# Kernel optimization log

Measured on AMD Instinct MI355X. Metric: run time of the kernel, lower is better.

## Reference

```python
import jax, jax.numpy as jnp
import numpy as np

B, T, I, H, OUT, L = 256, 1200, 16, 128, 1, 2


def _lstm_layer(x, W_ih, W_hh, b_ih, b_hh):
    # x: [B, T, Din]; W_ih: [4H, Din]; W_hh: [4H, H]
    # Precompute input contribution for all timesteps (one big GEMM),
    # then scan only the recurrent part.
    pre = jnp.einsum('btd,gd->btg', x, W_ih) + b_ih + b_hh  # [B, T, 4H]
    pre = jnp.swapaxes(pre, 0, 1)  # [T, B, 4H]
    h0 = jnp.zeros((x.shape[0], W_hh.shape[1]), dtype=x.dtype)
    c0 = jnp.zeros_like(h0)

    def step(carry, p_t):
        h, c = carry
        g = p_t + h @ W_hh.T  # [B, 4H]
        i, f, gg, o = jnp.split(g, 4, axis=-1)  # torch gate order: i, f, g, o
        i = jax.nn.sigmoid(i)
        f = jax.nn.sigmoid(f)
        gg = jnp.tanh(gg)
        o = jax.nn.sigmoid(o)
        c = f * c + i * gg
        h = o * jnp.tanh(c)
        return (h, c), h

    (_, _), hs = jax.lax.scan(step, (h0, c0), pre)  # hs: [T, B, H]
    return jnp.swapaxes(hs, 0, 1)  # [B, T, H]


def setup_inputs() -> dict:
    key = jax.random.key(0)
    ks = jax.random.split(key, 12)
    s = 0.08  # small init scale to keep gates unsaturated
    inp = {
        'x': jax.random.normal(ks[0], (B, T, I), dtype=jnp.float32),
        'W_ih0': jax.random.normal(ks[1], (4 * H, I), dtype=jnp.float32) * s,
        'W_hh0': jax.random.normal(ks[2], (4 * H, H), dtype=jnp.float32) * s,
        'b_ih0': jax.random.normal(ks[3], (4 * H,), dtype=jnp.float32) * s,
        'b_hh0': jax.random.normal(ks[4], (4 * H,), dtype=jnp.float32) * s,
        'W_ih1': jax.random.normal(ks[5], (4 * H, H), dtype=jnp.float32) * s,
        'W_hh1': jax.random.normal(ks[6], (4 * H, H), dtype=jnp.float32) * s,
        'b_ih1': jax.random.normal(ks[7], (4 * H,), dtype=jnp.float32) * s,
        'b_hh1': jax.random.normal(ks[8], (4 * H,), dtype=jnp.float32) * s,
        'W_lin': jax.random.normal(ks[9], (OUT, H), dtype=jnp.float32) * s,
        'b_lin': jax.random.normal(ks[10], (OUT,), dtype=jnp.float32) * s,
    }
    return inp


def reference(x, W_ih0, W_hh0, b_ih0, b_hh0, W_ih1, W_hh1, b_ih1, b_hh1, W_lin, b_lin):
    h1 = _lstm_layer(x, W_ih0, W_hh0, b_ih0, b_hh0)   # [B, T, H]
    h2 = _lstm_layer(h1, W_ih1, W_hh1, b_ih1, b_hh1)  # [B, T, H]
    out = jax.nn.relu(h2)
    out = jnp.einsum('bth,oh->bto', out, W_lin) + b_lin  # [B, T, OUT]
    return out.reshape(-1, 12)  # [B*T*OUT/12, 12]
```

## Files before the change

kernel.cpp:

```cpp
#include <hip/hip_runtime.h>
#include <hip/hip_fp16.h>

#define B_ 256
#define T_ 1200
#define I_ 16
#define H_ 128
#define NT_ (T_ / 8)

typedef __attribute__((ext_vector_type(2))) _Float16 h2;
typedef __attribute__((ext_vector_type(8))) _Float16 f16x8;

union f16x8u { f16x8 v; h2 h[4]; _Float16 s[8]; };

#if __has_builtin(__builtin_amdgcn_fdot2)
__device__ __forceinline__ float fdot2(h2 a, h2 b, float c) {
  return __builtin_amdgcn_fdot2(a, b, c, false);
}
#else
__device__ __forceinline__ float fdot2(h2 a, h2 b, float c) {
  return fmaf((float)a.x, (float)b.x, fmaf((float)a.y, (float)b.y, c));
}
#endif

template <int PAT>
__device__ __forceinline__ float qbcast(float x) {
  return __int_as_float(__builtin_amdgcn_update_dpp(0, __float_as_int(x), PAT, 0xF, 0xF, true));
}

__device__ __forceinline__ float wred(float x) {
  x += __int_as_float(__builtin_amdgcn_update_dpp(0, __float_as_int(x), 0x141, 0xF, 0xF, true));
  x += __int_as_float(__builtin_amdgcn_update_dpp(0, __float_as_int(x), 0x140, 0xF, 0xF, true));
  x += __shfl_xor(x, 16);
  x += __shfl_xor(x, 32);
  return x;
}

__device__ __forceinline__ float sigm(float x) {
  return __builtin_amdgcn_rcpf(1.f + __expf(-x));
}
__device__ __forceinline__ float tanh_(float x) {
  return 1.f - 2.f * __builtin_amdgcn_rcpf(1.f + __expf(2.f * x));
}

__device__ __forceinline__ void load_row_h2(const float* __restrict__ p, h2* w) {
#pragma unroll
  for (int i = 0; i < 32; ++i) {
    const float4 v = *(const float4*)(p + 4 * i);
    w[2 * i].x     = (_Float16)v.x; w[2 * i].y     = (_Float16)v.y;
    w[2 * i + 1].x = (_Float16)v.z; w[2 * i + 1].y = (_Float16)v.w;
  }
}

__global__ __launch_bounds__(512, 2) void k1_layer0(
    const float* __restrict__ xin,
    const float* __restrict__ Wih0, const float* __restrict__ Whh0,
    const float* __restrict__ bih0, const float* __restrict__ bhh0,
    __half* __restrict__ h0ws)
{
  __shared__ __align__(16) __half xs[T_ * I_];
  __shared__ __align__(16) __half hb[2][H_];

  const int tid = threadIdx.x;
  const int q = tid & 3;
  const int j = tid >> 2;
  const int g = q * H_ + j;
  const int b = blockIdx.x;

  {
    const float4* xg4 = (const float4*)(xin + (size_t)b * T_ * I_);
    for (int idx = tid; idx < T_ * I_ / 4; idx += 512) {
      const float4 v = xg4[idx];
      xs[4 * idx]     = __float2half(v.x);
      xs[4 * idx + 1] = __float2half(v.y);
      xs[4 * idx + 2] = __float2half(v.z);
      xs[4 * idx + 3] = __float2half(v.w);
    }
  }

  h2 wh[64], wx[8];
  load_row_h2(Whh0 + (size_t)g * H_, wh);
  {
    const float* px = Wih0 + (size_t)g * I_;
#pragma unroll
    for (int i = 0; i < 4; ++i) {
      const float4 v = *(const float4*)(px + 4 * i);
      wx[2 * i].x     = (_Float16)v.x; wx[2 * i].y     = (_Float16)v.y;
      wx[2 * i + 1].x = (_Float16)v.z; wx[2 * i + 1].y = (_Float16)v.w;
    }
  }
  const float bs = bih0[g] + bhh0[g];
  const float s0 = (q == 2) ? 1.f : 0.f;
  const float s1 = (q == 2) ? -2.f : 1.f;
  const float s2 = (q == 2) ? 2.f : -1.f;

  if (tid < H_) hb[0][tid] = __float2half(0.f);
  float cst = 0.f;
  __half* h0o = h0ws + (size_t)b * T_ * H_ + j;
  __syncthreads();

#pragma unroll 2
  for (int t = 0; t < T_; ++t) {
    const int rb = t & 1;
    float a0 = 0.f, a1 = 0.f, a2 = 0.f, a3 = 0.f;
#pragma unroll
    for (int i = 0; i < 16; ++i) {
      f16x8u u; u.v = *(const f16x8*)(&hb[rb][8 * i]);
      a0 = fdot2(wh[4 * i],     u.h[0], a0);
      a1 = fdot2(wh[4 * i + 1], u.h[1], a1);
      a2 = fdot2(wh[4 * i + 2], u.h[2], a2);
      a3 = fdot2(wh[4 * i + 3], u.h[3], a3);
    }
#pragma unroll
    for (int m = 0; m < 2; ++m) {
      f16x8u u; u.v = *(const f16x8*)(&xs[t * I_ + 8 * m]);
      a0 = fdot2(wx[4 * m],     u.h[0], a0);
      a1 = fdot2(wx[4 * m + 1], u.h[1], a1);
      a2 = fdot2(wx[4 * m + 2], u.h[2], a2);
      a3 = fdot2(wx[4 * m + 3], u.h[3], a3);
    }
    const float pre = (a0 + a1) + (a2 + a3) + bs;
    const float act = fmaf(s1, __builtin_amdgcn_rcpf(1.f + __expf(s2 * pre)), s0);
    const float ig = qbcast<0x00>(act);
    const float fg = qbcast<0x55>(act);
    const float gg = qbcast<0xAA>(act);
    const float og = qbcast<0xFF>(act);
    cst = fg * cst + ig * gg;
    const float hv = og * tanh_(cst);
    const __half hh = __float2half(hv);
    if (q == 0) {
      hb[rb ^ 1][j] = hh;
      h0o[(size_t)t * H_] = hh;
    }
    __syncthreads();
  }
}

__global__ __attribute__((amdgpu_waves_per_eu(4, 4)))
__launch_bounds__(1024) void kb_layer1(
    const __half* __restrict__ h0ws,
    const float* __restrict__ Wih1, const float* __restrict__ Whh1,
    const float* __restrict__ bih1, const float* __restrict__ bhh1,
    const float* __restrict__ Wlin, const float* __restrict__ blin,
    float* __restrict__ out)
{
  __shared__ __align__(16) __half h0til[2][8 * H_];
  __shared__ __align__(16) float aih[2][512];
  __shared__ __align__(16) __half h1b[2][H_];
  __shared__ __align__(16) float red[2][8];

  const int tid = threadIdx.x;
  const bool isA = tid < 512;
  const int lid = tid & 511;
  const int q = lid & 3;
  const int j = lid >> 2;
  const int g = q * H_ + j;
  const int b = blockIdx.x;

  h2 w[64];
  load_row_h2((isA ? Wih1 : Whh1) + (size_t)g * H_, w);

  const float bs = bih1[g] + bhh1[g];
  const float wl = Wlin[j];
  const float bl = blin[0];
  const float s0 = (q == 2) ? 1.f : 0.f;
  const float s1 = (q == 2) ? -2.f : 1.f;
  const float s2 = (q == 2) ? 2.f : -1.f;

  const uint* h0u = (const uint*)(h0ws + (size_t)b * T_ * H_);

  if (isA) ((uint*)h0til[0])[lid] = h0u[lid];
  if (!isA && lid < H_) h1b[0][lid] = __float2half(0.f);
  __syncthreads();
  if (isA) {
    float a0 = 0.f, a1 = 0.f, a2 = 0.f, a3 = 0.f;
#pragma unroll
    for (int i = 0; i < 16; ++i) {
      f16x8u u; u.v = *(const f16x8*)(&h0til[0][8 * i]);
      a0 = fdot2(w[4 * i],     u.h[0], a0);
      a1 = fdot2(w[4 * i + 1], u.h[1], a1);
      a2 = fdot2(w[4 * i + 2], u.h[2], a2);
      a3 = fdot2(w[4 * i + 3], u.h[3], a3);
    }
    aih[0][lid] = (a0 + a1) + (a2 + a3);
  }
  __syncthreads();

  float cst = 0.f;
  uint stg = 0;
  float* op = out + (size_t)b * T_;

  for (int t = 0; t < T_; ++t) {
    const int rb = t & 1;
    if (isA) {
      if ((t & 7) == 0) {
        const int m1 = (t >> 3) + 1;
        if (m1 < NT_) stg = h0u[m1 * 512 + lid];
      }
      const int tt = t + 1;
      if (tt < T_) {
        const __half* hsrc = &h0til[(tt >> 3) & 1][(tt & 7) * H_];
        float a0 = 0.f, a1 = 0.f, a2 = 0.f, a3 = 0.f;
#pragma unroll
        for (int i = 0; i < 16; ++i) {
          f16x8u u; u.v = *(const f16x8*)(hsrc + 8 * i);
          a0 = fdot2(w[4 * i],     u.h[0], a0);
          a1 = fdot2(w[4 * i + 1], u.h[1], a1);
          a2 = fdot2(w[4 * i + 2], u.h[2], a2);
          a3 = fdot2(w[4 * i + 3], u.h[3], a3);
        }
        aih[tt & 1][lid] = (a0 + a1) + (a2 + a3);
      }
      if ((t & 7) == 6) {
        const int m1 = (t >> 3) + 1;
        if (m1 < NT_) ((uint*)h0til[m1 & 1])[lid] = stg;
      }
    } else {
      float a0 = 0.f, a1 = 0.f, a2 = 0.f, a3 = 0.f;
#pragma unroll
      for (int i = 0; i < 16; ++i) {
        f16x8u u; u.v = *(const f16x8*)(&h1b[rb][8 * i]);
        a0 = fdot2(w[4 * i],     u.h[0], a0);
        a1 = fdot2(w[4 * i + 1], u.h[1], a1);
        a2 = fdot2(w[4 * i + 2], u.h[2], a2);
        a3 = fdot2(w[4 * i + 3], u.h[3], a3);
      }
      const float pre = (a0 + a1) + (a2 + a3) + aih[rb][lid] + bs;
      const float act = fmaf(s1, __builtin_amdgcn_rcpf(1.f + __expf(s2 * pre)), s0);
      const float ig = qbcast<0x00>(act);
      const float fg = qbcast<0x55>(act);
      const float gg = qbcast<0xAA>(act);
      const float og = qbcast<0xFF>(act);
      cst = fg * cst + ig * gg;
      const float hv = og * tanh_(cst);
      if (q == 0) h1b[rb ^ 1][j] = __float2half(hv);
      const float val = wred(fmaxf(hv, 0.f) * wl);
      if ((lid & 63) == 0) red[rb][lid >> 6] = val;
      if (t > 0 && lid == (((t - 1) & 7) << 6)) {
        const float4 r0 = *(const float4*)(&red[rb ^ 1][0]);
        const float4 r1 = *(const float4*)(&red[rb ^ 1][4]);
        op[t - 1] = bl + r0.x + r0.y + r0.z + r0.w + r1.x + r1.y + r1.z + r1.w;
      }
    }
    __syncthreads();
  }
  if (!isA && lid == (((T_ - 1) & 7) << 6)) {
    const float4 r0 = *(const float4*)(&red[(T_ - 1) & 1][0]);
    const float4 r1 = *(const float4*)(&red[(T_ - 1) & 1][4]);
    op[T_ - 1] = bl + r0.x + r0.y + r0.z + r0.w + r1.x + r1.y + r1.z + r1.w;
  }
}

__device__ __forceinline__ float qsum8f(float x) {
  x += __int_as_float(__builtin_amdgcn_update_dpp(0, __float_as_int(x), 0xB1, 0xF, 0xF, true));
  x += __int_as_float(__builtin_amdgcn_update_dpp(0, __float_as_int(x), 0x4E, 0xF, 0xF, true));
  return x;
}

__global__ __launch_bounds__(512, 2) void lstm_fused_fb(
    const float* __restrict__ xin,
    const float* __restrict__ Wih0, const float* __restrict__ Whh0,
    const float* __restrict__ bih0, const float* __restrict__ bhh0,
    const float* __restrict__ Wih1, const float* __restrict__ Whh1,
    const float* __restrict__ bih1, const float* __restrict__ bhh1,
    const float* __restrict__ Wlin, const float* __restrict__ blin,
    float* __restrict__ out)
{
  __shared__ __align__(16) __half buf0[2][H_];
  __shared__ __align__(16) __half buf1[2][H_];
  __shared__ __align__(16) float red[2][8];

  const int tid = threadIdx.x;
  const int c = tid & 3;
  const int j = tid >> 2;
  const int b = blockIdx.x;
  const int wv = tid >> 6;

  h2 w0[4][16], wi[4][16], wh[4][16];
  h2 wx[4][2];
  float bs0[4], bs1[4];

#pragma unroll
  for (int qq = 0; qq < 4; ++qq) {
    const int g = qq * H_ + j;
    const float* p0 = Whh0 + (size_t)g * H_ + c * 32;
    const float* p1 = Wih1 + (size_t)g * H_ + c * 32;
    const float* p2 = Whh1 + (size_t)g * H_ + c * 32;
#pragma unroll
    for (int i = 0; i < 8; ++i) {
      float4 v = *(const float4*)(p0 + 4 * i);
      w0[qq][2*i].x   = (_Float16)v.x; w0[qq][2*i].y   = (_Float16)v.y;
      w0[qq][2*i+1].x = (_Float16)v.z; w0[qq][2*i+1].y = (_Float16)v.w;
      v = *(const float4*)(p1 + 4 * i);
      wi[qq][2*i].x   = (_Float16)v.x; wi[qq][2*i].y   = (_Float16)v.y;
      wi[qq][2*i+1].x = (_Float16)v.z; wi[qq][2*i+1].y = (_Float16)v.w;
      v = *(const float4*)(p2 + 4 * i);
      wh[qq][2*i].x   = (_Float16)v.x; wh[qq][2*i].y   = (_Float16)v.y;
      wh[qq][2*i+1].x = (_Float16)v.z; wh[qq][2*i+1].y = (_Float16)v.w;
    }
    const float4 vx = *(const float4*)(Wih0 + (size_t)g * I_ + 4 * c);
    wx[qq][0].x = (_Float16)vx.x; wx[qq][0].y = (_Float16)vx.y;
    wx[qq][1].x = (_Float16)vx.z; wx[qq][1].y = (_Float16)vx.w;
    bs0[qq] = bih0[g] + bhh0[g];
    bs1[qq] = bih1[g] + bhh1[g];
  }
  const float wl = Wlin[j];
  const float bl = blin[0];

  if (tid < H_) {
    buf0[0][tid] = __float2half(0.f);
    buf1[0][tid] = __float2half(0.f);
  }
  float cst0 = 0.f, cst1 = 0.f;
  const float* xp = xin + (size_t)b * T_ * I_ + 4 * c;
  float* op = out + (size_t)b * T_;
  __syncthreads();

#pragma unroll 2
  for (int t = 0; t < T_; ++t) {
    const int rb = t & 1;
    const float4 xv = *(const float4*)xp; xp += I_;
    float a0 = 0.f, a1 = 0.f, a2 = 0.f, a3 = 0.f;
#pragma unroll
    for (int i = 0; i < 4; ++i) {
      f16x8u u; u.v = *(const f16x8*)(&buf0[rb][c * 32 + i * 8]);
#pragma unroll
      for (int p = 0; p < 4; ++p) {
        const h2 hv = u.h[p];
        a0 = fdot2(w0[0][4 * i + p], hv, a0);
        a1 = fdot2(w0[1][4 * i + p], hv, a1);
        a2 = fdot2(w0[2][4 * i + p], hv, a2);
        a3 = fdot2(w0[3][4 * i + p], hv, a3);
      }
    }
    h2 xa, xb;
    xa.x = (_Float16)xv.x; xa.y = (_Float16)xv.y;
    xb.x = (_Float16)xv.z; xb.y = (_Float16)xv.w;
    a0 = fdot2(wx[0][0], xa, fdot2(wx[0][1], xb, a0));
    a1 = fdot2(wx[1][0], xa, fdot2(wx[1][1], xb, a1));
    a2 = fdot2(wx[2][0], xa, fdot2(wx[2][1], xb, a2));
    a3 = fdot2(wx[3][0], xa, fdot2(wx[3][1], xb, a3));
    {
      const float g0 = qsum8f(a0) + bs0[0];
      const float g1 = qsum8f(a1) + bs0[1];
      const float g2 = qsum8f(a2) + bs0[2];
      const float g3 = qsum8f(a3) + bs0[3];
      const float ig = sigm(g0), fg = sigm(g1), gg = tanh_(g2), og = sigm(g3);
      cst0 = fg * cst0 + ig * gg;
      const float h0v = og * tanh_(cst0);
      if (c == 0) buf0[rb ^ 1][j] = __float2half(h0v);
    }
    __syncthreads();
    a0 = 0.f; a1 = 0.f; a2 = 0.f; a3 = 0.f;
#pragma unroll
    for (int i = 0; i < 4; ++i) {
      f16x8u u; u.v = *(const f16x8*)(&buf0[rb ^ 1][c * 32 + i * 8]);
#pragma unroll
      for (int p = 0; p < 4; ++p) {
        const h2 hv = u.h[p];
        a0 = fdot2(wi[0][4 * i + p], hv, a0);
        a1 = fdot2(wi[1][4 * i + p], hv, a1);
        a2 = fdot2(wi[2][4 * i + p], hv, a2);
        a3 = fdot2(wi[3][4 * i + p], hv, a3);
      }
    }
#pragma unroll
    for (int i = 0; i < 4; ++i) {
      f16x8u u; u.v = *(const f16x8*)(&buf1[rb][c * 32 + i * 8]);
#pragma unroll
      for (int p = 0; p < 4; ++p) {
        const h2 hv = u.h[p];
        a0 = fdot2(wh[0][4 * i + p], hv, a0);
        a1 = fdot2(wh[1][4 * i + p], hv, a1);
        a2 = fdot2(wh[2][4 * i + p], hv, a2);
        a3 = fdot2(wh[3][4 * i + p], hv, a3);
      }
    }
    const float g0 = qsum8f(a0) + bs1[0];
    const float g1 = qsum8f(a1) + bs1[1];
    const float g2 = qsum8f(a2) + bs1[2];
    const float g3 = qsum8f(a3) + bs1[3];
    const float ig = sigm(g0), fg = sigm(g1), gg = tanh_(g2), og = sigm(g3);
    cst1 = fg * cst1 + ig * gg;
    const float h1v = og * tanh_(cst1);
    if (c == 0) buf1[rb ^ 1][j] = __float2half(h1v);
    float val = wred(fmaxf(h1v, 0.f) * wl);
    if ((tid & 63) == 0) red[rb][wv] = val;
    __syncthreads();
    if (tid == ((t & 7) << 6)) {
      const float4 r0 = *(const float4*)(&red[rb][0]);
      const float4 r1 = *(const float4*)(&red[rb][4]);
      op[t] = bl + r0.x + r0.y + r0.z + r0.w + r1.x + r1.y + r1.z + r1.w;
    }
  }
}

extern "C" void kernel_launch(void* const* d_in, const int* in_sizes, int n_in,
                              void* d_out, int out_size, void* d_ws, size_t ws_size,
                              hipStream_t stream) {
  const size_t H0_BYTES = (size_t)B_ * T_ * H_ * sizeof(__half);

  if (d_ws != nullptr && ws_size >= H0_BYTES) {
    __half* h0ws = (__half*)d_ws;
    k1_layer0<<<B_, 512, 0, stream>>>(
        (const float*)d_in[0],
        (const float*)d_in[1], (const float*)d_in[2],
        (const float*)d_in[3], (const float*)d_in[4],
        h0ws);
    kb_layer1<<<B_, 1024, 0, stream>>>(
        h0ws,
        (const float*)d_in[5], (const float*)d_in[6],
        (const float*)d_in[7], (const float*)d_in[8],
        (const float*)d_in[9], (const float*)d_in[10],
        (float*)d_out);
  } else {
    lstm_fused_fb<<<B_, 512, 0, stream>>>(
        (const float*)d_in[0],
        (const float*)d_in[1], (const float*)d_in[2],
        (const float*)d_in[3], (const float*)d_in[4],
        (const float*)d_in[5], (const float*)d_in[6],
        (const float*)d_in[7], (const float*)d_in[8],
        (const float*)d_in[9], (const float*)d_in[10],
        (float*)d_out);
  }
}
```

Before: 1.927 ms.

## Merge layer-1 producer/consumer waves into one 512-thread block with LDS input weights

Layer 1 used to run as a 1024-thread block in which half the threads precomputed the input projection for the next step while the other half ran the recurrence. The new kernel uses 512 threads, each computing both the input and recurrent dot products within the same step. The input weights move to padded LDS, and the recurrent weights stay in registers. This removes the aih exchange through shared memory and may allow two blocks per CU, but it puts the input GEMV on the serial critical path and adds an LDS weight read every step. The fallback kernel's sigmoid helper is also replaced by an inline division.

```diff
diff --git a/kernel.cpp b/kernel.cpp
--- a/kernel.cpp
+++ b/kernel.cpp
@@ -35,9 +35,6 @@
   return x;
 }
 
-__device__ __forceinline__ float sigm(float x) {
-  return __builtin_amdgcn_rcpf(1.f + __expf(-x));
-}
 __device__ __forceinline__ float tanh_(float x) {
   return 1.f - 2.f * __builtin_amdgcn_rcpf(1.f + __expf(2.f * x));
 }
@@ -135,30 +132,37 @@
   }
 }
 
-__global__ __attribute__((amdgpu_waves_per_eu(4, 4)))
-__launch_bounds__(1024) void kb_layer1(
+__global__ __launch_bounds__(512, 2) void kl1_layer1(
     const __half* __restrict__ h0ws,
     const float* __restrict__ Wih1, const float* __restrict__ Whh1,
     const float* __restrict__ bih1, const float* __restrict__ bhh1,
     const float* __restrict__ Wlin, const float* __restrict__ blin,
     float* __restrict__ out)
 {
+  __shared__ __align__(16) __half wi_l[512][130];
   __shared__ __align__(16) __half h0til[2][8 * H_];
-  __shared__ __align__(16) float aih[2][512];
   __shared__ __align__(16) __half h1b[2][H_];
   __shared__ __align__(16) float red[2][8];
 
   const int tid = threadIdx.x;
-  const bool isA = tid < 512;
-  const int lid = tid & 511;
-  const int q = lid & 3;
-  const int j = lid >> 2;
+  const int q = tid & 3;
+  const int j = tid >> 2;
   const int g = q * H_ + j;
   const int b = blockIdx.x;
 
-  h2 w[64];
-  load_row_h2((isA ? Wih1 : Whh1) + (size_t)g * H_, w);
-
+  {
+    const float* src = Wih1 + (size_t)g * H_;
+#pragma unroll
+    for (int i = 0; i < 32; ++i) {
+      const float4 v = *(const float4*)(src + 4 * i);
+      __half* dst = &wi_l[tid][4 * i];
+      dst[0] = __float2half(v.x); dst[1] = __float2half(v.y);
+      dst[2] = __float2half(v.z); dst[3] = __float2half(v.w);
+    }
+  }
+
+  h2 wh[64];
+  load_row_h2(Whh1 + (size_t)g * H_, wh);
   const float bs = bih1[g] + bhh1[g];
   const float wl = Wlin[j];
   const float bl = blin[0];
@@ -167,83 +171,63 @@
   const float s2 = (q == 2) ? 2.f : -1.f;
 
   const uint* h0u = (const uint*)(h0ws + (size_t)b * T_ * H_);
-
-  if (isA) ((uint*)h0til[0])[lid] = h0u[lid];
-  if (!isA && lid < H_) h1b[0][lid] = __float2half(0.f);
-  __syncthreads();
-  if (isA) {
-    float a0 = 0.f, a1 = 0.f, a2 = 0.f, a3 = 0.f;
-#pragma unroll
-    for (int i = 0; i < 16; ++i) {
-      f16x8u u; u.v = *(const f16x8*)(&h0til[0][8 * i]);
-      a0 = fdot2(w[4 * i],     u.h[0], a0);
-      a1 = fdot2(w[4 * i + 1], u.h[1], a1);
-      a2 = fdot2(w[4 * i + 2], u.h[2], a2);
-      a3 = fdot2(w[4 * i + 3], u.h[3], a3);
-    }
-    aih[0][lid] = (a0 + a1) + (a2 + a3);
-  }
-  __syncthreads();
-
+  ((uint*)h0til[0])[tid] = h0u[tid];
+  if (tid < H_) h1b[0][tid] = __float2half(0.f);
   float cst = 0.f;
   uint stg = 0;
   float* op = out + (size_t)b * T_;
-
+  __syncthreads();
+
+#pragma unroll 1
   for (int t = 0; t < T_; ++t) {
     const int rb = t & 1;
-    if (isA) {
-      if ((t & 7) == 0) {
-        const int m1 = (t >> 3) + 1;
-        if (m1 < NT_) stg = h0u[m1 * 512 + lid];
-      }
-      const int tt = t + 1;
-      if (tt < T_) {
-        const __half* hsrc = &h0til[(tt >> 3) & 1][(tt & 7) * H_];
-        float a0 = 0.f, a1 = 0.f, a2 = 0.f, a3 = 0.f;
-#pragma unroll
-        for (int i = 0; i < 16; ++i) {
-          f16x8u u; u.v = *(const f16x8*)(hsrc + 8 * i);
-          a0 = fdot2(w[4 * i],     u.h[0], a0);
-          a1 = fdot2(w[4 * i + 1], u.h[1], a1);
-          a2 = fdot2(w[4 * i + 2], u.h[2], a2);
-          a3 = fdot2(w[4 * i + 3], u.h[3], a3);
-        }
-        aih[tt & 1][lid] = (a0 + a1) + (a2 + a3);
-      }
-      if ((t & 7) == 6) {
-        const int m1 = (t >> 3) + 1;
-        if (m1 < NT_) ((uint*)h0til[m1 & 1])[lid] = stg;
-      }
-    } else {
-      float a0 = 0.f, a1 = 0.f, a2 = 0.f, a3 = 0.f;
-#pragma unroll
-      for (int i = 0; i < 16; ++i) {
-        f16x8u u; u.v = *(const f16x8*)(&h1b[rb][8 * i]);
-        a0 = fdot2(w[4 * i],     u.h[0], a0);
-        a1 = fdot2(w[4 * i + 1], u.h[1], a1);
-        a2 = fdot2(w[4 * i + 2], u.h[2], a2);
-        a3 = fdot2(w[4 * i + 3], u.h[3], a3);
-      }
-      const float pre = (a0 + a1) + (a2 + a3) + aih[rb][lid] + bs;
-      const float act = fmaf(s1, __builtin_amdgcn_rcpf(1.f + __expf(s2 * pre)), s0);
-      const float ig = qbcast<0x00>(act);
-      const float fg = qbcast<0x55>(act);
-      const float gg = qbcast<0xAA>(act);
-      const float og = qbcast<0xFF>(act);
-      cst = fg * cst + ig * gg;
-      const float hv = og * tanh_(cst);
-      if (q == 0) h1b[rb ^ 1][j] = __float2half(hv);
-      const float val = wred(fmaxf(hv, 0.f) * wl);
-      if ((lid & 63) == 0) red[rb][lid >> 6] = val;
-      if (t > 0 && lid == (((t - 1) & 7) << 6)) {
-        const float4 r0 = *(const float4*)(&red[rb ^ 1][0]);
-        const float4 r1 = *(const float4*)(&red[rb ^ 1][4]);
-        op[t - 1] = bl + r0.x + r0.y + r0.z + r0.w + r1.x + r1.y + r1.z + r1.w;
-      }
+    if ((t & 7) == 0) {
+      const int m1 = (t >> 3) + 1;
+      if (m1 < NT_) stg = h0u[m1 * 512 + tid];
+    }
+    const __half* hsrc = &h0til[(t >> 3) & 1][(t & 7) * H_];
+    float a0 = 0.f, a1 = 0.f, a2 = 0.f, a3 = 0.f;
+#pragma unroll
+    for (int i = 0; i < 16; ++i) {
+      f16x8u uw; uw.v = *(const f16x8*)(&wi_l[tid][8 * i]);
+      f16x8u uh; uh.v = *(const f16x8*)(hsrc + 8 * i);
+      a0 = fdot2(uw.h[0], uh.h[0], a0);
+      a1 = fdot2(uw.h[1], uh.h[1], a1);
+      a2 = fdot2(uw.h[2], uh.h[2], a2);
+      a3 = fdot2(uw.h[3], uh.h[3], a3);
+    }
+    float c0 = 0.f, c1 = 0.f, c2 = 0.f, c3 = 0.f;
+#pragma unroll
+    for (int i = 0; i < 16; ++i) {
+      f16x8u uh; uh.v = *(const f16x8*)(&h1b[rb][8 * i]);
+      c0 = fdot2(wh[4 * i],     uh.h[0], c0);
+      c1 = fdot2(wh[4 * i + 1], uh.h[1], c1);
+      c2 = fdot2(wh[4 * i + 2], uh.h[2], c2);
+      c3 = fdot2(wh[4 * i + 3], uh.h[3], c3);
+    }
+    if ((t & 7) == 6) {
+      const int m1 = (t >> 3) + 1;
+      if (m1 < NT_) ((uint*)h0til[m1 & 1])[tid] = stg;
+    }
+    const float pre = ((a0 + a1) + (a2 + a3)) + ((c0 + c1) + (c2 + c3)) + bs;
+    const float act = fmaf(s1, __builtin_amdgcn_rcpf(1.f + __expf(s2 * pre)), s0);
+    const float ig = qbcast<0x00>(act);
+    const float fg = qbcast<0x55>(act);
+    const float gg = qbcast<0xAA>(act);
+    const float og = qbcast<0xFF>(act);
+    cst = fg * cst + ig * gg;
+    const float hv = og * tanh_(cst);
+    if (q == 0) h1b[rb ^ 1][j] = __float2half(hv);
+    const float val = wred(fmaxf(hv, 0.f) * wl);
+    if ((tid & 63) == 0) red[rb][tid >> 6] = val;
+    if (t > 0 && tid == (((t - 1) & 7) << 6)) {
+      const float4 r0 = *(const float4*)(&red[rb ^ 1][0]);
+      const float4 r1 = *(const float4*)(&red[rb ^ 1][4]);
+      op[t - 1] = bl + r0.x + r0.y + r0.z + r0.w + r1.x + r1.y + r1.z + r1.w;
     }
     __syncthreads();
   }
-  if (!isA && lid == (((T_ - 1) & 7) << 6)) {
+  if (tid == (((T_ - 1) & 7) << 6)) {
     const float4 r0 = *(const float4*)(&red[(T_ - 1) & 1][0]);
     const float4 r1 = *(const float4*)(&red[(T_ - 1) & 1][4]);
     op[T_ - 1] = bl + r0.x + r0.y + r0.z + r0.w + r1.x + r1.y + r1.z + r1.w;
@@ -344,7 +328,10 @@
       const float g1 = qsum8f(a1) + bs0[1];
       const float g2 = qsum8f(a2) + bs0[2];
       const float g3 = qsum8f(a3) + bs0[3];
-      const float ig = sigm(g0), fg = sigm(g1), gg = tanh_(g2), og = sigm(g3);
+      const float ig = 1.f / (1.f + __expf(-g0));
+      const float fg = 1.f / (1.f + __expf(-g1));
+      const float gg = tanh_(g2);
+      const float og = 1.f / (1.f + __expf(-g3));
       cst0 = fg * cst0 + ig * gg;
       const float h0v = og * tanh_(cst0);
       if (c == 0) buf0[rb ^ 1][j] = __float2half(h0v);
@@ -379,7 +366,10 @@
     const float g1 = qsum8f(a1) + bs1[1];
     const float g2 = qsum8f(a2) + bs1[2];
     const float g3 = qsum8f(a3) + bs1[3];
-    const float ig = sigm(g0), fg = sigm(g1), gg = tanh_(g2), og = sigm(g3);
+    const float ig = 1.f / (1.f + __expf(-g0));
+    const float fg = 1.f / (1.f + __expf(-g1));
+    const float gg = tanh_(g2);
+    const float og = 1.f / (1.f + __expf(-g3));
     cst1 = fg * cst1 + ig * gg;
     const float h1v = og * tanh_(cst1);
     if (c == 0) buf1[rb ^ 1][j] = __float2half(h1v);
@@ -406,7 +396,7 @@
         (const float*)d_in[1], (const float*)d_in[2],
         (const float*)d_in[3], (const float*)d_in[4],
         h0ws);
-    kb_layer1<<<B_, 1024, 0, stream>>>(
+    kl1_layer1<<<B_, 512, 0, stream>>>(
         h0ws,
         (const float*)d_in[5], (const float*)d_in[6],
         (const float*)d_in[7], (const float*)d_in[8],
```

New measurement: 4.186 ms. 2.17x slower.
